# Performance work log

Measured on AMD Instinct MI355X. Metric: run time of the kernel, lower is better.

Reference implementation:

```python
import jax, jax.numpy as jnp
import numpy as np

N_NODES = 100000
N_EDGES = 1600000
FEAT = 128
HID = 128
N_CLASSES = 18
N_CENT = 2
N_GRAPHS = 512
AC_STD_LIM = 5.0
RUNNING_MEAN = 1.0
RUNNING_VAR = 0.0


def setup_inputs() -> dict:
    key = jax.random.key(0)
    ks = jax.random.split(key, 12)
    x = jax.random.normal(ks[0], (N_NODES, FEAT), jnp.float32)
    edge_index = jax.random.randint(ks[1], (2, N_EDGES), 0, N_NODES, dtype=jnp.int64)
    batch = jnp.sort(jax.random.randint(ks[2], (N_NODES,), 0, N_GRAPHS, dtype=jnp.int64))
    def glorot(k, fan_in, fan_out):
        lim = float(np.sqrt(6.0 / (fan_in + fan_out)))
        return jax.random.uniform(k, (fan_in, fan_out), jnp.float32, -lim, lim)
    W1 = glorot(ks[3], FEAT, HID); b1 = jnp.zeros((HID,), jnp.float32)
    W2 = glorot(ks[4], HID, HID); b2 = jnp.zeros((HID,), jnp.float32)
    W3 = glorot(ks[5], HID, HID); b3 = jnp.zeros((HID,), jnp.float32)
    centroids = jax.random.normal(ks[6], (N_CLASSES, N_CENT, HID), jnp.float32)
    std_scale = jnp.array(1.0, jnp.float32)
    ac_temp = jnp.array(1.0, jnp.float32)
    return dict(x=x, edge_index=edge_index, batch=batch,
                W1=W1, b1=b1, W2=W2, b2=b2, W3=W3, b3=b3,
                centroids=centroids, std_scale=std_scale, ac_temp=ac_temp)


def gcn_conv(x, W, b, src, dst, n_nodes):
    # PyG GCNConv: h = x @ W, symmetric normalization with self-loops, then + b
    h = x @ W
    ones = jnp.ones(src.shape[0], h.dtype)
    deg = jax.ops.segment_sum(ones, dst, num_segments=n_nodes) + 1.0  # +1 self-loop
    dinv = jax.lax.rsqrt(deg)
    norm = dinv[src] * dinv[dst]                      # [E]
    msg = h[src] * norm[:, None]                      # gather + scale  [E, H]
    agg = jax.ops.segment_sum(msg, dst, num_segments=n_nodes)
    agg = agg + h * (1.0 / deg)[:, None]              # self-loop contribution (deg^-1)
    return agg + b


def reference(x, edge_index, batch, W1, b1, W2, b2, W3, b3, centroids, std_scale, ac_temp):
    src, dst = edge_index[0], edge_index[1]
    n = x.shape[0]
    h = jax.nn.relu(gcn_conv(x, W1, b1, src, dst, n))   # dropout inactive (eval)
    h = jax.nn.relu(gcn_conv(h, W2, b2, src, dst, n))
    h = gcn_conv(h, W3, b3, src, dst, n)
    # global mean pool over graphs
    sums = jax.ops.segment_sum(h, batch, num_segments=N_GRAPHS)
    cnt = jax.ops.segment_sum(jnp.ones(n, h.dtype), batch, num_segments=N_GRAPHS)
    g = sums / jnp.maximum(cnt, 1.0)[:, None]           # [B, H]
    # CentroidLayer (reject_input=True, eval mode: running stats frozen)
    diff = centroids[None] - g[:, None, None]           # [B, C, n_cent, H]
    dist = jnp.min(jnp.sqrt(jnp.sum(diff * diff, axis=-1)), axis=2)  # [B, C]
    y = -dist
    max_ac = RUNNING_MEAN + jnp.clip(jax.nn.relu(std_scale), 0.0, AC_STD_LIM) * jnp.sqrt(RUNNING_VAR)
    accept = max_ac - jax.lax.stop_gradient(jnp.min(dist, axis=1, keepdims=True))
    soft = jax.nn.sigmoid(accept / ac_temp)             # [B, 1]
    out = jnp.concatenate([y, soft], axis=1)            # [B, C+1]
    return out[:, :-1], out[:, -1]
```

## Files before the change

### kernel.cpp

```cpp
#include <hip/hip_runtime.h>
#include <hip/hip_bf16.h>
#include <math.h>

#define NN 100000
#define NEDGE 1600000
#define HIDF 128
#define NCLS 18
#define NGR 512
#define CHSZ 2048
#define NBKT 391

using bf16x8  = __attribute__((ext_vector_type(8))) short;
using ushort8 = __attribute__((ext_vector_type(8))) unsigned short;
using f32x4   = __attribute__((ext_vector_type(4))) float;
using f32x2   = __attribute__((ext_vector_type(2))) float;

__device__ __forceinline__ float b2f(unsigned short u) {
    return __uint_as_float(((unsigned)u) << 16);
}
__device__ __forceinline__ unsigned short f2b(float f) {
    unsigned u = __float_as_uint(f);
    unsigned r = (u + 0x7fffu + ((u >> 16) & 1u)) >> 16;
    return (unsigned short)r;
}
__device__ __forceinline__ unsigned char f2fp8(float f) {
    int p = __builtin_amdgcn_cvt_pk_fp8_f32(f, f, 0, false);
    return (unsigned char)(p & 0xff);
}

__global__ __launch_bounds__(256) void bin_kernel(const int* __restrict__ src,
                                                  const int* __restrict__ dst,
                                                  long long* __restrict__ recs_out,
                                                  int2* __restrict__ cando, int nE) {
    __shared__ int cnt[512];
    __shared__ int ssum[256];
    __shared__ long long recs[CHSZ];
    int c = blockIdx.x;
    int t = threadIdx.x;
    cnt[t] = 0; cnt[t + 256] = 0;
    __syncthreads();
    int e0 = c * CHSZ;
    int nv = nE - e0; if (nv > CHSZ) nv = CHSZ;
    int s8[8], d8[8];
    #pragma unroll
    for (int i = 0; i < 8; i++) {
        int li = t + i * 256;
        bool ok = li < nv;
        s8[i] = ok ? src[e0 + li] : -1;
        d8[i] = ok ? dst[e0 + li] : -1;
        if (ok) atomicAdd(&cnt[d8[i] >> 8], 1);
    }
    __syncthreads();
    int a = cnt[2 * t], b_ = cnt[2 * t + 1];
    ssum[t] = a + b_;
    __syncthreads();
    for (int off = 1; off < 256; off <<= 1) {
        int v = (t >= off) ? ssum[t - off] : 0;
        __syncthreads();
        ssum[t] += v;
        __syncthreads();
    }
    int excl = ssum[t] - (a + b_);
    if (2 * t < NBKT)     cando[(size_t)c * NBKT + 2 * t]     = make_int2(a, excl);
    if (2 * t + 1 < NBKT) cando[(size_t)c * NBKT + 2 * t + 1] = make_int2(b_, excl + a);
    __syncthreads();
    cnt[2 * t] = excl; cnt[2 * t + 1] = excl + a;
    __syncthreads();
    #pragma unroll
    for (int i = 0; i < 8; i++) {
        if (d8[i] >= 0) {
            int pos = atomicAdd(&cnt[d8[i] >> 8], 1);
            recs[pos] = ((long long)d8[i] << 32) | (unsigned)s8[i];
        }
    }
    __syncthreads();
    for (int j = t; j < nv; j += 256)
        recs_out[(size_t)e0 + j] = recs[j];
}

__global__ __launch_bounds__(512) void bucket_count_kernel(const long long* __restrict__ recs_bin,
                                                           const int2* __restrict__ cando,
                                                           int* __restrict__ cnt,
                                                           int* __restrict__ bktsum,
                                                           float* __restrict__ dinv,
                                                           float* __restrict__ selfw,
                                                           int nch, int n) {
    __shared__ int c256[256];
    __shared__ int wsum[4];
    int b = blockIdx.x;
    int t = threadIdx.x;
    if (t < 256) c256[t] = 0;
    __syncthreads();
    for (int c = t; c < nch; c += 512) {
        int2 co = cando[(size_t)c * NBKT + b];
        size_t base = (size_t)c * CHSZ + co.y;
        for (int k = 0; k < co.x; ++k) {
            long long rec = recs_bin[base + k];
            int d = (int)(rec >> 32);
            atomicAdd(&c256[d & 255], 1);
        }
    }
    __syncthreads();
    int node = (b << 8) + t;
    int cv = 0;
    if (t < 256) {
        cv = c256[t];
        if (node < n) {
            cnt[node] = cv;
            float deg = (float)cv + 1.0f;
            dinv[node]  = rsqrtf(deg);
            selfw[node] = 1.0f / deg;
        }
    }
    if (t < 256) {
        int s = cv;
        #pragma unroll
        for (int off = 32; off > 0; off >>= 1) s += __shfl_down(s, off);
        if ((t & 63) == 0) wsum[t >> 6] = s;
    }
    __syncthreads();
    if (t == 0) bktsum[b] = wsum[0] + wsum[1] + wsum[2] + wsum[3];
}

__global__ __launch_bounds__(512) void scan_bkt_kernel(const int* __restrict__ bktsum,
                                                       int* __restrict__ bktoff, int nb) {
    __shared__ int t512[512];
    int t = threadIdx.x;
    t512[t] = (t < nb) ? bktsum[t] : 0;
    __syncthreads();
    for (int off = 1; off < 512; off <<= 1) {
        int v = (t >= off) ? t512[t - off] : 0;
        __syncthreads();
        t512[t] += v;
        __syncthreads();
    }
    if (t < nb) bktoff[t] = (t == 0) ? 0 : t512[t - 1];
}

__global__ __launch_bounds__(512) void bucket_fill_kernel(const long long* __restrict__ recs_bin,
                                                          const int2* __restrict__ cando,
                                                          const int* __restrict__ cnt,
                                                          const int* __restrict__ bktoff,
                                                          const float* __restrict__ dinv,
                                                          int* __restrict__ rowptr,
                                                          long long* __restrict__ csr_rec,
                                                          int nch, int n, int nE) {
    __shared__ int cur[256];
    __shared__ int scn[256];
    int b = blockIdx.x;
    int node0 = b << 8;
    int t = threadIdx.x;
    int cv = 0;
    if (t < 256) {
        int nd = node0 + t;
        cv = (nd < n) ? cnt[nd] : 0;
        scn[t] = cv;
    }
    __syncthreads();
    for (int off = 1; off < 256; off <<= 1) {
        int v = (t < 256 && t >= off) ? scn[t - off] : 0;
        __syncthreads();
        if (t < 256) scn[t] += v;
        __syncthreads();
    }
    if (t < 256) {
        int nd = node0 + t;
        int excl = bktoff[b] + scn[t] - cv;
        if (nd < n) { rowptr[nd] = excl; cur[t] = excl; }
    }
    if (b == NBKT - 1 && t == 0) rowptr[n] = nE;
    __syncthreads();
    for (int c = t; c < nch; c += 512) {
        int2 co = cando[(size_t)c * NBKT + b];
        size_t base = (size_t)c * CHSZ + co.y;
        for (int k = 0; k < co.x; ++k) {
            long long rec = recs_bin[base + k];
            int d = (int)(rec >> 32);
            int s = (int)(unsigned)(rec & 0xffffffffLL);
            float w = dinv[s] * dinv[d];
            int pos = atomicAdd(&cur[d & 255], 1);
            csr_rec[pos] = ((long long)__float_as_int(w) << 32) | (unsigned)s;
        }
    }
}

__global__ __launch_bounds__(256) void wprep_kernel(const float* __restrict__ W1,
                                                    const float* __restrict__ W2,
                                                    const float* __restrict__ W3,
                                                    unsigned short* __restrict__ Wf) {
    int gid = blockIdx.x * 256 + threadIdx.x;
    int w = gid >> 14;
    int o = gid & 16383;
    int j = o & 7, lane = (o >> 3) & 63, ct = (o >> 9) & 7, kt = o >> 12;
    int rk = kt * 32 + (lane >> 4) * 8 + j;
    int col = ct * 16 + (lane & 15);
    const float* W = (w == 0) ? W1 : ((w == 1) ? W2 : W3);
    Wf[gid] = f2b(W[rk * HIDF + col]);
}

__global__ __launch_bounds__(256) void mfma_gemm_kernel(const float* __restrict__ X,
                                                        const unsigned short* __restrict__ Wfrag,
                                                        unsigned char* __restrict__ Hfp8, int n) {
    __shared__ unsigned short wl[16384];
    {
        const uint4* wsrc = reinterpret_cast<const uint4*>(Wfrag);
        uint4* wdst = reinterpret_cast<uint4*>(wl);
        for (int i = threadIdx.x; i < 2048; i += 256) wdst[i] = wsrc[i];
    }
    __syncthreads();

    int wv = threadIdx.x >> 6;
    int l  = threadIdx.x & 63;
    int row = blockIdx.x * 64 + wv * 16 + (l & 15);
    int koff = (l >> 4) * 8;
    bool rowok = row < n;

    f32x4 acc[8] = {};
    #pragma unroll
    for (int kt = 0; kt < 4; ++kt) {
        int kbase = kt * 32 + koff;
        bf16x8 a;
        float4 x0 = {0,0,0,0}, x1 = {0,0,0,0};
        if (rowok) {
            x0 = *reinterpret_cast<const float4*>(&X[(size_t)row * HIDF + kbase]);
            x1 = *reinterpret_cast<const float4*>(&X[(size_t)row * HIDF + kbase + 4]);
        }
        a[0] = (short)f2b(x0.x); a[1] = (short)f2b(x0.y);
        a[2] = (short)f2b(x0.z); a[3] = (short)f2b(x0.w);
        a[4] = (short)f2b(x1.x); a[5] = (short)f2b(x1.y);
        a[6] = (short)f2b(x1.z); a[7] = (short)f2b(x1.w);
        #pragma unroll
        for (int ct = 0; ct < 8; ++ct) {
            bf16x8 b = *reinterpret_cast<bf16x8*>(&wl[((kt * 8 + ct) * 64 + l) * 8]);
            acc[ct] = __builtin_amdgcn_mfma_f32_16x16x32_bf16(a, b, acc[ct], 0, 0, 0);
        }
    }
    int rbase = blockIdx.x * 64 + wv * 16 + ((l >> 4) << 2);
    int cbase = l & 15;
    #pragma unroll
    for (int ct = 0; ct < 8; ++ct) {
        #pragma unroll
        for (int r = 0; r < 4; ++r) {
            int gr = rbase + r;
            if (gr < n) Hfp8[(size_t)gr * HIDF + ct * 16 + cbase] = f2fp8(acc[ct][r]);
        }
    }
}

__global__ __launch_bounds__(512) void fused_gather_gemm_kernel(
        const unsigned char* __restrict__ Hin,
        const int* __restrict__ rowptr,
        const long long* __restrict__ csr_rec,
        const float* __restrict__ selfw,
        const float* __restrict__ bias,
        const unsigned short* __restrict__ Wfrag,
        unsigned char* __restrict__ Hout, int n) {
    __shared__ unsigned short wl[16384];
    __shared__ unsigned short agg[64][136];
    {
        const uint4* wsrc = reinterpret_cast<const uint4*>(Wfrag);
        uint4* wdst = reinterpret_cast<uint4*>(wl);
        for (int i = threadIdx.x; i < 2048; i += 512) wdst[i] = wsrc[i];
    }
    int node0 = blockIdx.x * 64;
    int nl   = threadIdx.x >> 3;
    int node = node0 + nl;
    int lane = threadIdx.x & 7;
    if (node < n) {
        float acc[16];
        {
            uint4 sv = *reinterpret_cast<const uint4*>(Hin + (size_t)node * HIDF + lane * 16);
            const unsigned* svw = reinterpret_cast<const unsigned*>(&sv);
            float sw = selfw[node];
            #pragma unroll
            for (int d = 0; d < 4; ++d) {
                f32x2 lo = __builtin_amdgcn_cvt_pk_f32_fp8((int)svw[d], false);
                f32x2 hi = __builtin_amdgcn_cvt_pk_f32_fp8((int)svw[d], true);
                acc[d * 4 + 0] = lo[0] * sw; acc[d * 4 + 1] = lo[1] * sw;
                acc[d * 4 + 2] = hi[0] * sw; acc[d * 4 + 3] = hi[1] * sw;
            }
        }
        int beg = rowptr[node], end = rowptr[node + 1];
        int nfull = (end - beg) >> 3;
        int base = beg;
        for (int fb = 0; fb < nfull; ++fb, base += 8) {
            long long rec = csr_rec[base + lane];
            uint4 v[8];
            float w[8];
            #pragma unroll
            for (int j = 0; j < 8; ++j) {
                long long r = __shfl(rec, j, 8);
                int sn = (int)(unsigned)(r & 0xffffffffLL);
                w[j] = __int_as_float((int)(r >> 32));
                v[j] = *reinterpret_cast<const uint4*>(Hin + (size_t)sn * HIDF + lane * 16);
            }
            #pragma unroll
            for (int j = 0; j < 8; ++j) {
                const unsigned* vw = reinterpret_cast<const unsigned*>(&v[j]);
                #pragma unroll
                for (int d = 0; d < 4; ++d) {
                    f32x2 lo = __builtin_amdgcn_cvt_pk_f32_fp8((int)vw[d], false);
                    f32x2 hi = __builtin_amdgcn_cvt_pk_f32_fp8((int)vw[d], true);
                    acc[d * 4 + 0] += lo[0] * w[j]; acc[d * 4 + 1] += lo[1] * w[j];
                    acc[d * 4 + 2] += hi[0] * w[j]; acc[d * 4 + 3] += hi[1] * w[j];
                }
            }
        }
        int m = end - base;
        if (m > 0) {
            long long rec = (base + lane < end) ? csr_rec[base + lane] : 0;
            for (int j = 0; j < m; ++j) {
                long long r = __shfl(rec, j, 8);
                int sn = (int)(unsigned)(r & 0xffffffffLL);
                float w = __int_as_float((int)(r >> 32));
                uint4 v = *reinterpret_cast<const uint4*>(Hin + (size_t)sn * HIDF + lane * 16);
                const unsigned* vw = reinterpret_cast<const unsigned*>(&v);
                #pragma unroll
                for (int d = 0; d < 4; ++d) {
                    f32x2 lo = __builtin_amdgcn_cvt_pk_f32_fp8((int)vw[d], false);
                    f32x2 hi = __builtin_amdgcn_cvt_pk_f32_fp8((int)vw[d], true);
                    acc[d * 4 + 0] += lo[0] * w; acc[d * 4 + 1] += lo[1] * w;
                    acc[d * 4 + 2] += hi[0] * w; acc[d * 4 + 3] += hi[1] * w;
                }
            }
        }
        #pragma unroll
        for (int i = 0; i < 16; ++i) {
            float vb = acc[i] + bias[lane * 16 + i];
            agg[nl][lane * 16 + i] = f2b(fmaxf(vb, 0.f));
        }
    } else {
        #pragma unroll
        for (int i = 0; i < 16; ++i) agg[nl][lane * 16 + i] = 0;
    }
    __syncthreads();
    int wv = threadIdx.x >> 6;
    int l  = threadIdx.x & 63;
    int mt  = wv >> 1;
    int ct0 = (wv & 1) * 4;
    int arow = mt * 16 + (l & 15);
    int koff = (l >> 4) * 8;
    f32x4 acc4[4] = {};
    #pragma unroll
    for (int kt = 0; kt < 4; ++kt) {
        int kbase = kt * 32 + koff;
        bf16x8 a = *reinterpret_cast<bf16x8*>(&agg[arow][kbase]);
        #pragma unroll
        for (int c = 0; c < 4; ++c) {
            int ct = ct0 + c;
            bf16x8 b = *reinterpret_cast<bf16x8*>(&wl[((kt * 8 + ct) * 64 + l) * 8]);
            acc4[c] = __builtin_amdgcn_mfma_f32_16x16x32_bf16(a, b, acc4[c], 0, 0, 0);
        }
    }
    int rloc = mt * 16 + ((l >> 4) << 2);
    int cbase = l & 15;
    #pragma unroll
    for (int c = 0; c < 4; ++c) {
        int ct = ct0 + c;
        #pragma unroll
        for (int r = 0; r < 4; ++r) {
            int gr = node0 + rloc + r;
            if (gr < n) Hout[(size_t)gr * HIDF + ct * 16 + cbase] = f2fp8(acc4[c][r]);
        }
    }
}

__global__ __launch_bounds__(256) void gather_agg_kernel(const unsigned char* __restrict__ Hin,
                                                         const int* __restrict__ rowptr,
                                                         const long long* __restrict__ csr_rec,
                                                         const float* __restrict__ selfw,
                                                         unsigned short* __restrict__ Hout, int n) {
    int node = blockIdx.x * 32 + (threadIdx.x >> 3);
    if (node >= n) return;
    int lane = threadIdx.x & 7;
    float acc[16];
    {
        uint4 sv = *reinterpret_cast<const uint4*>(Hin + (size_t)node * HIDF + lane * 16);
        const unsigned* svw = reinterpret_cast<const unsigned*>(&sv);
        float sw = selfw[node];
        #pragma unroll
        for (int d = 0; d < 4; ++d) {
            f32x2 lo = __builtin_amdgcn_cvt_pk_f32_fp8((int)svw[d], false);
            f32x2 hi = __builtin_amdgcn_cvt_pk_f32_fp8((int)svw[d], true);
            acc[d * 4 + 0] = lo[0] * sw; acc[d * 4 + 1] = lo[1] * sw;
            acc[d * 4 + 2] = hi[0] * sw; acc[d * 4 + 3] = hi[1] * sw;
        }
    }
    int beg = rowptr[node], end = rowptr[node + 1];
    int nfull = (end - beg) >> 3;
    int base = beg;
    for (int fb = 0; fb < nfull; ++fb, base += 8) {
        long long rec = csr_rec[base + lane];
        uint4 v[8];
        float w[8];
        #pragma unroll
        for (int j = 0; j < 8; ++j) {
            long long r = __shfl(rec, j, 8);
            int sn = (int)(unsigned)(r & 0xffffffffLL);
            w[j] = __int_as_float((int)(r >> 32));
            v[j] = *reinterpret_cast<const uint4*>(Hin + (size_t)sn * HIDF + lane * 16);
        }
        #pragma unroll
        for (int j = 0; j < 8; ++j) {
            const unsigned* vw = reinterpret_cast<const unsigned*>(&v[j]);
            #pragma unroll
            for (int d = 0; d < 4; ++d) {
                f32x2 lo = __builtin_amdgcn_cvt_pk_f32_fp8((int)vw[d], false);
                f32x2 hi = __builtin_amdgcn_cvt_pk_f32_fp8((int)vw[d], true);
                acc[d * 4 + 0] += lo[0] * w[j]; acc[d * 4 + 1] += lo[1] * w[j];
                acc[d * 4 + 2] += hi[0] * w[j]; acc[d * 4 + 3] += hi[1] * w[j];
            }
        }
    }
    int m = end - base;
    if (m > 0) {
        long long rec = (base + lane < end) ? csr_rec[base + lane] : 0;
        for (int j = 0; j < m; ++j) {
            long long r = __shfl(rec, j, 8);
            int sn = (int)(unsigned)(r & 0xffffffffLL);
            float w = __int_as_float((int)(r >> 32));
            uint4 v = *reinterpret_cast<const uint4*>(Hin + (size_t)sn * HIDF + lane * 16);
            const unsigned* vw = reinterpret_cast<const unsigned*>(&v);
            #pragma unroll
            for (int d = 0; d < 4; ++d) {
                f32x2 lo = __builtin_amdgcn_cvt_pk_f32_fp8((int)vw[d], false);
                f32x2 hi = __builtin_amdgcn_cvt_pk_f32_fp8((int)vw[d], true);
                acc[d * 4 + 0] += lo[0] * w; acc[d * 4 + 1] += lo[1] * w;
                acc[d * 4 + 2] += hi[0] * w; acc[d * 4 + 3] += hi[1] * w;
            }
        }
    }
    ushort8 o0, o1;
    #pragma unroll
    for (int i = 0; i < 8; ++i) o0[i] = f2b(acc[i]);
    #pragma unroll
    for (int i = 0; i < 8; ++i) o1[i] = f2b(acc[8 + i]);
    unsigned short* op = Hout + (size_t)node * HIDF + lane * 16;
    *reinterpret_cast<ushort8*>(op) = o0;
    *reinterpret_cast<ushort8*>(op + 8) = o1;
}

__device__ __forceinline__ int lower_bound_i(const int* __restrict__ a, int n, int key) {
    int lo = 0, hi = n;
    while (lo < hi) { int mid = (lo + hi) >> 1; if (a[mid] < key) lo = mid + 1; else hi = mid; }
    return lo;
}

__global__ __launch_bounds__(256) void pool_final_kernel(const unsigned short* __restrict__ H,
                                                         const int* __restrict__ batch,
                                                         const float* __restrict__ b3,
                                                         const float* __restrict__ centroids,
                                                         const float* __restrict__ std_scale,
                                                         const float* __restrict__ ac_temp,
                                                         float* __restrict__ out, int n) {
    __shared__ float part[8][HIDF];
    __shared__ float gm[HIDF];
    int b = blockIdx.x;
    int g = threadIdx.x >> 5;
    int lane = threadIdx.x & 31;
    int s = lower_bound_i(batch, n, b);
    int e = lower_bound_i(batch, n, b + 1);
    float4 acc = {0.f, 0.f, 0.f, 0.f};
    for (int i = s + g; i < e; i += 8) {
        ushort4 v = *reinterpret_cast<const ushort4*>(&H[(size_t)i * HIDF + lane * 4]);
        acc.x += b2f(v.x); acc.y += b2f(v.y);
        acc.z += b2f(v.z); acc.w += b2f(v.w);
    }
    part[g][lane * 4 + 0] = acc.x;
    part[g][lane * 4 + 1] = acc.y;
    part[g][lane * 4 + 2] = acc.z;
    part[g][lane * 4 + 3] = acc.w;
    __syncthreads();
    if (threadIdx.x < HIDF) {
        int f = threadIdx.x;
        float sum = 0.f;
        #pragma unroll
        for (int gg = 0; gg < 8; ++gg) sum += part[gg][f];
        float cnt = fmaxf((float)(e - s), 1.0f);
        gm[f] = sum / cnt + b3[f];
    }
    __syncthreads();
    if (threadIdx.x < 64) {
        int l = threadIdx.x;
        float g0 = gm[l];
        float g1 = gm[64 + l];
        float mind = 1e30f;
        for (int c = 0; c < NCLS; ++c) {
            float dd[2];
            #pragma unroll
            for (int cent = 0; cent < 2; ++cent) {
                const float* cp = &centroids[(c * 2 + cent) * HIDF];
                float df0 = cp[l] - g0;
                float df1 = cp[64 + l] - g1;
                float p = df0 * df0 + df1 * df1;
                #pragma unroll
                for (int off = 32; off > 0; off >>= 1) p += __shfl_xor(p, off);
                dd[cent] = p;
            }
            float dist = fminf(sqrtf(dd[0]), sqrtf(dd[1]));
            mind = fminf(mind, dist);
            if (l == 0) out[b * NCLS + c] = -dist;
        }
        if (l == 0) {
            float ss = std_scale[0];
            float clipped = fminf(fmaxf(ss, 0.0f), 5.0f);
            float max_ac = 1.0f + clipped * 0.0f;
            float accept = max_ac - mind;
            float soft = 1.0f / (1.0f + expf(-accept / ac_temp[0]));
            out[NGR * NCLS + b] = soft;
        }
    }
}

extern "C" void kernel_launch(void* const* d_in, const int* in_sizes, int n_in,
                              void* d_out, int out_size, void* d_ws, size_t ws_size,
                              hipStream_t stream) {
    const float* x         = (const float*)d_in[0];
    const int*   edge      = (const int*)d_in[1];
    const int*   batch     = (const int*)d_in[2];
    const float* W1        = (const float*)d_in[3];
    const float* b1        = (const float*)d_in[4];
    const float* W2        = (const float*)d_in[5];
    const float* b2        = (const float*)d_in[6];
    const float* W3        = (const float*)d_in[7];
    const float* b3        = (const float*)d_in[8];
    const float* centroids = (const float*)d_in[9];
    const float* std_scale = (const float*)d_in[10];
    const float* ac_temp   = (const float*)d_in[11];
    float* out = (float*)d_out;

    const int n  = NN;
    const int nE = in_sizes[1] / 2;
    const int* srcp = edge;
    const int* dstp = edge + nE;
    const int nch = (nE + CHSZ - 1) / CHSZ;

    char* ws = (char*)d_ws;
    size_t off = 0;
    auto alloc = [&](size_t bytes) { void* p = ws + off; off = (off + bytes + 255) & ~(size_t)255; return p; };
    unsigned char*  hP = (unsigned char*) alloc((size_t)NN * HIDF);
    unsigned char*  hQ = (unsigned char*) alloc((size_t)NN * HIDF);
    unsigned short* hG = (unsigned short*)alloc((size_t)NN * HIDF * 2);
    unsigned short* Wf = (unsigned short*)alloc((size_t)3 * HIDF * HIDF * 2);
    float* dinv    = (float*)alloc((size_t)NN * 4);
    float* selfw   = (float*)alloc((size_t)NN * 4);
    int*   cnt     = (int*)  alloc((size_t)NN * 4);
    int*   rowptr  = (int*)  alloc((size_t)(NN + 1) * 4);
    long long* csr_rec  = (long long*)alloc((size_t)nE * 8);
    long long* recs_bin = (long long*)alloc((size_t)nE * 8);
    int2*  cando   = (int2*) alloc((size_t)nch * NBKT * 8);
    int*   bktsum  = (int*)  alloc((size_t)NBKT * 4);
    int*   bktoff  = (int*)  alloc((size_t)NBKT * 4);

    wprep_kernel<<<192, 256, 0, stream>>>(W1, W2, W3, Wf);
    bin_kernel<<<nch, 256, 0, stream>>>(srcp, dstp, recs_bin, cando, nE);
    bucket_count_kernel<<<NBKT, 512, 0, stream>>>(recs_bin, cando, cnt, bktsum, dinv, selfw, nch, n);
    scan_bkt_kernel<<<1, 512, 0, stream>>>(bktsum, bktoff, NBKT);
    bucket_fill_kernel<<<NBKT, 512, 0, stream>>>(recs_bin, cando, cnt, bktoff, dinv, rowptr, csr_rec, nch, n, nE);

    int gemm_blocks  = (n + 63) / 64;
    int fused_blocks = (n + 63) / 64;
    int gath_blocks  = (n + 31) / 32;

    mfma_gemm_kernel<<<gemm_blocks, 256, 0, stream>>>(x, Wf, hP, n);
    fused_gather_gemm_kernel<<<fused_blocks, 512, 0, stream>>>(hP, rowptr, csr_rec, selfw, b1, Wf + 16384, hQ, n);
    fused_gather_gemm_kernel<<<fused_blocks, 512, 0, stream>>>(hQ, rowptr, csr_rec, selfw, b2, Wf + 32768, hP, n);
    gather_agg_kernel<<<gath_blocks, 256, 0, stream>>>(hP, rowptr, csr_rec, selfw, hG, n);
    pool_final_kernel<<<NGR, 256, 0, stream>>>(hG, batch, b3, centroids, std_scale, ac_temp, out, n);
}
```

Measured before the change: 244.0 us.

## Fuse final-layer gather into per-graph pooling and read W fragments from global

```diff
diff --git a/kernel.cpp b/kernel.cpp
--- a/kernel.cpp
+++ b/kernel.cpp
@@ -255,13 +255,7 @@
         const float* __restrict__ bias,
         const unsigned short* __restrict__ Wfrag,
         unsigned char* __restrict__ Hout, int n) {
-    __shared__ unsigned short wl[16384];
     __shared__ unsigned short agg[64][136];
-    {
-        const uint4* wsrc = reinterpret_cast<const uint4*>(Wfrag);
-        uint4* wdst = reinterpret_cast<uint4*>(wl);
-        for (int i = threadIdx.x; i < 2048; i += 512) wdst[i] = wsrc[i];
-    }
     int node0 = blockIdx.x * 64;
     int nl   = threadIdx.x >> 3;
     int node = node0 + nl;
@@ -348,7 +342,7 @@
         #pragma unroll
         for (int c = 0; c < 4; ++c) {
             int ct = ct0 + c;
-            bf16x8 b = *reinterpret_cast<bf16x8*>(&wl[((kt * 8 + ct) * 64 + l) * 8]);
+            bf16x8 b = *reinterpret_cast<const bf16x8*>(&Wfrag[((kt * 8 + ct) * 64 + l) * 8]);
             acc4[c] = __builtin_amdgcn_mfma_f32_16x16x32_bf16(a, b, acc4[c], 0, 0, 0);
         }
     }
@@ -363,81 +357,6 @@
             if (gr < n) Hout[(size_t)gr * HIDF + ct * 16 + cbase] = f2fp8(acc4[c][r]);
         }
     }
-}
-
-__global__ __launch_bounds__(256) void gather_agg_kernel(const unsigned char* __restrict__ Hin,
-                                                         const int* __restrict__ rowptr,
-                                                         const long long* __restrict__ csr_rec,
-                                                         const float* __restrict__ selfw,
-                                                         unsigned short* __restrict__ Hout, int n) {
-    int node = blockIdx.x * 32 + (threadIdx.x >> 3);
-    if (node >= n) return;
-    int lane = threadIdx.x & 7;
-    float acc[16];
-    {
-        uint4 sv = *reinterpret_cast<const uint4*>(Hin + (size_t)node * HIDF + lane * 16);
-        const unsigned* svw = reinterpret_cast<const unsigned*>(&sv);
-        float sw = selfw[node];
-        #pragma unroll
-        for (int d = 0; d < 4; ++d) {
-            f32x2 lo = __builtin_amdgcn_cvt_pk_f32_fp8((int)svw[d], false);
-            f32x2 hi = __builtin_amdgcn_cvt_pk_f32_fp8((int)svw[d], true);
-            acc[d * 4 + 0] = lo[0] * sw; acc[d * 4 + 1] = lo[1] * sw;
-            acc[d * 4 + 2] = hi[0] * sw; acc[d * 4 + 3] = hi[1] * sw;
-        }
-    }
-    int beg = rowptr[node], end = rowptr[node + 1];
-    int nfull = (end - beg) >> 3;
-    int base = beg;
-    for (int fb = 0; fb < nfull; ++fb, base += 8) {
-        long long rec = csr_rec[base + lane];
-        uint4 v[8];
-        float w[8];
-        #pragma unroll
-        for (int j = 0; j < 8; ++j) {
-            long long r = __shfl(rec, j, 8);
-            int sn = (int)(unsigned)(r & 0xffffffffLL);
-            w[j] = __int_as_float((int)(r >> 32));
-            v[j] = *reinterpret_cast<const uint4*>(Hin + (size_t)sn * HIDF + lane * 16);
-        }
-        #pragma unroll
-        for (int j = 0; j < 8; ++j) {
-            const unsigned* vw = reinterpret_cast<const unsigned*>(&v[j]);
-            #pragma unroll
-            for (int d = 0; d < 4; ++d) {
-                f32x2 lo = __builtin_amdgcn_cvt_pk_f32_fp8((int)vw[d], false);
-                f32x2 hi = __builtin_amdgcn_cvt_pk_f32_fp8((int)vw[d], true);
-                acc[d * 4 + 0] += lo[0] * w[j]; acc[d * 4 + 1] += lo[1] * w[j];
-                acc[d * 4 + 2] += hi[0] * w[j]; acc[d * 4 + 3] += hi[1] * w[j];
-            }
-        }
-    }
-    int m = end - base;
-    if (m > 0) {
-        long long rec = (base + lane < end) ? csr_rec[base + lane] : 0;
-        for (int j = 0; j < m; ++j) {
-            long long r = __shfl(rec, j, 8);
-            int sn = (int)(unsigned)(r & 0xffffffffLL);
-            float w = __int_as_float((int)(r >> 32));
-            uint4 v = *reinterpret_cast<const uint4*>(Hin + (size_t)sn * HIDF + lane * 16);
-            const unsigned* vw = reinterpret_cast<const unsigned*>(&v);
-            #pragma unroll
-            for (int d = 0; d < 4; ++d) {
-                f32x2 lo = __builtin_amdgcn_cvt_pk_f32_fp8((int)vw[d], false);
-                f32x2 hi = __builtin_amdgcn_cvt_pk_f32_fp8((int)vw[d], true);
-                acc[d * 4 + 0] += lo[0] * w; acc[d * 4 + 1] += lo[1] * w;
-                acc[d * 4 + 2] += hi[0] * w; acc[d * 4 + 3] += hi[1] * w;
-            }
-        }
-    }
-    ushort8 o0, o1;
-    #pragma unroll
-    for (int i = 0; i < 8; ++i) o0[i] = f2b(acc[i]);
-    #pragma unroll
-    for (int i = 0; i < 8; ++i) o1[i] = f2b(acc[8 + i]);
-    unsigned short* op = Hout + (size_t)node * HIDF + lane * 16;
-    *reinterpret_cast<ushort8*>(op) = o0;
-    *reinterpret_cast<ushort8*>(op + 8) = o1;
 }
 
 __device__ __forceinline__ int lower_bound_i(const int* __restrict__ a, int n, int key) {
@@ -446,36 +365,96 @@
     return lo;
 }
 
-__global__ __launch_bounds__(256) void pool_final_kernel(const unsigned short* __restrict__ H,
-                                                         const int* __restrict__ batch,
-                                                         const float* __restrict__ b3,
-                                                         const float* __restrict__ centroids,
-                                                         const float* __restrict__ std_scale,
-                                                         const float* __restrict__ ac_temp,
-                                                         float* __restrict__ out, int n) {
-    __shared__ float part[8][HIDF];
+__global__ __launch_bounds__(512) void gather_pool_final_kernel(
+        const unsigned char* __restrict__ Hin,
+        const int* __restrict__ rowptr,
+        const long long* __restrict__ csr_rec,
+        const float* __restrict__ selfw,
+        const int* __restrict__ batch,
+        const float* __restrict__ b3,
+        const float* __restrict__ centroids,
+        const float* __restrict__ std_scale,
+        const float* __restrict__ ac_temp,
+        float* __restrict__ out, int n) {
+    __shared__ float part[64][HIDF];
     __shared__ float gm[HIDF];
     int b = blockIdx.x;
-    int g = threadIdx.x >> 5;
-    int lane = threadIdx.x & 31;
+    int grp  = threadIdx.x >> 3;
+    int lane = threadIdx.x & 7;
     int s = lower_bound_i(batch, n, b);
     int e = lower_bound_i(batch, n, b + 1);
-    float4 acc = {0.f, 0.f, 0.f, 0.f};
-    for (int i = s + g; i < e; i += 8) {
-        ushort4 v = *reinterpret_cast<const ushort4*>(&H[(size_t)i * HIDF + lane * 4]);
-        acc.x += b2f(v.x); acc.y += b2f(v.y);
-        acc.z += b2f(v.z); acc.w += b2f(v.w);
-    }
-    part[g][lane * 4 + 0] = acc.x;
-    part[g][lane * 4 + 1] = acc.y;
-    part[g][lane * 4 + 2] = acc.z;
-    part[g][lane * 4 + 3] = acc.w;
+    float acc[16];
+    #pragma unroll
+    for (int i = 0; i < 16; ++i) acc[i] = 0.f;
+    for (int node = s + grp; node < e; node += 64) {
+        float t[16];
+        {
+            uint4 sv = *reinterpret_cast<const uint4*>(Hin + (size_t)node * HIDF + lane * 16);
+            const unsigned* svw = reinterpret_cast<const unsigned*>(&sv);
+            float sw = selfw[node];
+            #pragma unroll
+            for (int d = 0; d < 4; ++d) {
+                f32x2 lo = __builtin_amdgcn_cvt_pk_f32_fp8((int)svw[d], false);
+                f32x2 hi = __builtin_amdgcn_cvt_pk_f32_fp8((int)svw[d], true);
+                t[d * 4 + 0] = lo[0] * sw; t[d * 4 + 1] = lo[1] * sw;
+                t[d * 4 + 2] = hi[0] * sw; t[d * 4 + 3] = hi[1] * sw;
+            }
+        }
+        int beg = rowptr[node], end = rowptr[node + 1];
+        int nfull = (end - beg) >> 3;
+        int base = beg;
+        for (int fb = 0; fb < nfull; ++fb, base += 8) {
+            long long rec = csr_rec[base + lane];
+            uint4 v[8];
+            float w[8];
+            #pragma unroll
+            for (int j = 0; j < 8; ++j) {
+                long long r = __shfl(rec, j, 8);
+                int sn = (int)(unsigned)(r & 0xffffffffLL);
+                w[j] = __int_as_float((int)(r >> 32));
+                v[j] = *reinterpret_cast<const uint4*>(Hin + (size_t)sn * HIDF + lane * 16);
+            }
+            #pragma unroll
+            for (int j = 0; j < 8; ++j) {
+                const unsigned* vw = reinterpret_cast<const unsigned*>(&v[j]);
+                #pragma unroll
+                for (int d = 0; d < 4; ++d) {
+                    f32x2 lo = __builtin_amdgcn_cvt_pk_f32_fp8((int)vw[d], false);
+                    f32x2 hi = __builtin_amdgcn_cvt_pk_f32_fp8((int)vw[d], true);
+                    t[d * 4 + 0] += lo[0] * w[j]; t[d * 4 + 1] += lo[1] * w[j];
+                    t[d * 4 + 2] += hi[0] * w[j]; t[d * 4 + 3] += hi[1] * w[j];
+                }
+            }
+        }
+        int m = end - base;
+        if (m > 0) {
+            long long rec = (base + lane < end) ? csr_rec[base + lane] : 0;
+            for (int j = 0; j < m; ++j) {
+                long long r = __shfl(rec, j, 8);
+                int sn = (int)(unsigned)(r & 0xffffffffLL);
+                float w = __int_as_float((int)(r >> 32));
+                uint4 v = *reinterpret_cast<const uint4*>(Hin + (size_t)sn * HIDF + lane * 16);
+                const unsigned* vw = reinterpret_cast<const unsigned*>(&v);
+                #pragma unroll
+                for (int d = 0; d < 4; ++d) {
+                    f32x2 lo = __builtin_amdgcn_cvt_pk_f32_fp8((int)vw[d], false);
+                    f32x2 hi = __builtin_amdgcn_cvt_pk_f32_fp8((int)vw[d], true);
+                    t[d * 4 + 0] += lo[0] * w; t[d * 4 + 1] += lo[1] * w;
+                    t[d * 4 + 2] += hi[0] * w; t[d * 4 + 3] += hi[1] * w;
+                }
+            }
+        }
+        #pragma unroll
+        for (int i = 0; i < 16; ++i) acc[i] += t[i];
+    }
+    #pragma unroll
+    for (int i = 0; i < 16; ++i) part[grp][lane * 16 + i] = acc[i];
     __syncthreads();
     if (threadIdx.x < HIDF) {
         int f = threadIdx.x;
         float sum = 0.f;
-        #pragma unroll
-        for (int gg = 0; gg < 8; ++gg) sum += part[gg][f];
+        #pragma unroll 8
+        for (int g = 0; g < 64; ++g) sum += part[g][f];
         float cnt = fmaxf((float)(e - s), 1.0f);
         gm[f] = sum / cnt + b3[f];
     }
@@ -540,7 +519,6 @@
     auto alloc = [&](size_t bytes) { void* p = ws + off; off = (off + bytes + 255) & ~(size_t)255; return p; };
     unsigned char*  hP = (unsigned char*) alloc((size_t)NN * HIDF);
     unsigned char*  hQ = (unsigned char*) alloc((size_t)NN * HIDF);
-    unsigned short* hG = (unsigned short*)alloc((size_t)NN * HIDF * 2);
     unsigned short* Wf = (unsigned short*)alloc((size_t)3 * HIDF * HIDF * 2);
     float* dinv    = (float*)alloc((size_t)NN * 4);
     float* selfw   = (float*)alloc((size_t)NN * 4);
@@ -560,11 +538,10 @@
 
     int gemm_blocks  = (n + 63) / 64;
     int fused_blocks = (n + 63) / 64;
-    int gath_blocks  = (n + 31) / 32;
 
     mfma_gemm_kernel<<<gemm_blocks, 256, 0, stream>>>(x, Wf, hP, n);
     fused_gather_gemm_kernel<<<fused_blocks, 512, 0, stream>>>(hP, rowptr, csr_rec, selfw, b1, Wf + 16384, hQ, n);
     fused_gather_gemm_kernel<<<fused_blocks, 512, 0, stream>>>(hQ, rowptr, csr_rec, selfw, b2, Wf + 32768, hP, n);
-    gather_agg_kernel<<<gath_blocks, 256, 0, stream>>>(hP, rowptr, csr_rec, selfw, hG, n);
-    pool_final_kernel<<<NGR, 256, 0, stream>>>(hG, batch, b3, centroids, std_scale, ac_temp, out, n);
-}
+    gather_pool_final_kernel<<<NGR, 512, 0, stream>>>(hP, rowptr, csr_rec, selfw, batch, b3,
+                                                      centroids, std_scale, ac_temp, out, n);
+}
```

New measurement: 232.4 us. 4.8% less time.
